# Kernel tuning notes

Measured on AMD Instinct MI355X. Metric: run time of the kernel, lower is better.

## Reference

```python
import jax, jax.numpy as jnp
import numpy as np
import math

HEADS = 32
GROUPS = 8
HEAD_DIM = 64
HIDDEN = 2048
B, S = 2, 2048


def _rope(x, freqs_cis):
    # x: (..., S, head_dim); freqs_cis: (S, head_dim) -> interleaved cos/sin pattern
    x_even = x[..., ::2]
    x_odd = x[..., 1::2]
    cos = freqs_cis[..., ::2]
    sin = freqs_cis[..., 1::2]
    r_even = x_even * cos - x_odd * sin
    r_odd = x_even * sin + x_odd * cos
    return jnp.stack([r_even, r_odd], axis=-1).reshape(x.shape)


def setup_inputs() -> dict:
    key = jax.random.key(0)
    ks = jax.random.split(key, 12)
    scale = 1.0 / math.sqrt(HIDDEN)
    x = jax.random.normal(ks[0], (B, S, HIDDEN), dtype=jnp.float32)
    freqs_cis = jax.random.uniform(ks[1], (S, HEAD_DIM), dtype=jnp.float32)
    causal = jnp.tril(jnp.ones((S, S), dtype=bool))
    mask = jnp.where(causal, 0.0, -1e9).astype(jnp.float32)
    kv_dims = HEAD_DIM * GROUPS
    wq = jax.random.normal(ks[2], (HIDDEN, HIDDEN), jnp.float32) * scale
    bq = jnp.zeros((HIDDEN,), jnp.float32)
    wk = jax.random.normal(ks[3], (kv_dims, HIDDEN), jnp.float32) * scale
    bk = jnp.zeros((kv_dims,), jnp.float32)
    wv = jax.random.normal(ks[4], (kv_dims, HIDDEN), jnp.float32) * scale
    bv = jnp.zeros((kv_dims,), jnp.float32)
    wo = jax.random.normal(ks[5], (HIDDEN, HIDDEN), jnp.float32) * scale
    bo = jnp.zeros((HIDDEN,), jnp.float32)
    return dict(x=x, freqs_cis=freqs_cis, mask=mask, wq=wq, bq=bq,
                wk=wk, bk=bk, wv=wv, bv=bv, wo=wo, bo=bo)


def reference(x, freqs_cis, mask, wq, bq, wk, bk, wv, bv, wo, bo):
    b, s, h = x.shape
    rep = HEADS // GROUPS
    q = x @ wq.T + bq                      # (B,S,H)
    k = x @ wk.T + bk                      # (B,S,G*hd)
    v = x @ wv.T + bv
    q = q.reshape(b, s, HEADS, HEAD_DIM).transpose(0, 2, 1, 3)   # (B,Hh,S,hd)
    k = k.reshape(b, s, GROUPS, HEAD_DIM).transpose(0, 2, 1, 3)  # (B,G,S,hd)
    v = v.reshape(b, s, GROUPS, HEAD_DIM).transpose(0, 2, 1, 3)
    q = _rope(q, freqs_cis)
    k = _rope(k, freqs_cis)
    # GQA: group q heads instead of materially repeating K/V
    qg = q.reshape(b, GROUPS, rep, s, HEAD_DIM)
    scores = jnp.einsum('bgrsd,bgtd->bgrst', qg, k) / math.sqrt(HEAD_DIM)
    scores = scores + mask                 # broadcast (S,S)
    attn = jax.nn.softmax(scores, axis=-1)
    out = jnp.einsum('bgrst,bgtd->bgrsd', attn, v)
    out = out.reshape(b, HEADS, s, HEAD_DIM).transpose(0, 2, 1, 3).reshape(b, s, h)
    return out @ wo.T + bo
```

## Files before the change

### kernel.cpp

```cpp
#include <hip/hip_runtime.h>

#define S_LEN 2048
#define HID   2048
#define NQH   32
#define NKV   8
#define HD    64

typedef __bf16 bf16x8 __attribute__((ext_vector_type(8)));
typedef __bf16 bf16x4 __attribute__((ext_vector_type(4)));
typedef float  f32x4  __attribute__((ext_vector_type(4)));

#define MFMA16(a, b, c) __builtin_amdgcn_mfma_f32_16x16x32_bf16(a, b, c, 0, 0, 0)

__device__ __forceinline__ void async_copy16(const void* g, void* l) {
  __builtin_amdgcn_global_load_lds(
      (const __attribute__((address_space(1))) unsigned int*)g,
      (__attribute__((address_space(3))) unsigned int*)l, 16, 0, 0);
}

__global__ void cast_all_k(const float* __restrict__ x,  const float* __restrict__ wq,
                           const float* __restrict__ wk, const float* __restrict__ wv,
                           const float* __restrict__ wo,
                           __bf16* __restrict__ xb,  __bf16* __restrict__ wqb,
                           __bf16* __restrict__ wkb, __bf16* __restrict__ wvb,
                           __bf16* __restrict__ wob) {
  int bid = blockIdx.x;
  const float* in; __bf16* out; int base;
  if (bid < 8192)       { in = x;  out = xb;  base = bid; }
  else if (bid < 12288) { in = wq; out = wqb; base = bid - 8192; }
  else if (bid < 13312) { in = wk; out = wkb; base = bid - 12288; }
  else if (bid < 14336) { in = wv; out = wvb; base = bid - 13312; }
  else                  { in = wo; out = wob; base = bid - 14336; }
  int i = (base * 256 + threadIdx.x) * 4;
  float4 v = *(const float4*)(in + i);
  bf16x4 o;
  o[0] = (__bf16)v.x; o[1] = (__bf16)v.y; o[2] = (__bf16)v.z; o[3] = (__bf16)v.w;
  *(bf16x4*)(out + i) = o;
}

__device__ __forceinline__ void gemm_core(const __bf16* __restrict__ A, const __bf16* __restrict__ B,
                                          int m0, int n0, int K,
                                          __bf16 (&Asm)[128][32], __bf16 (&Bsm)[128][32],
                                          f32x4 (&acc)[4][4]) {
  const int tid = threadIdx.x, wave = tid >> 6, lane = tid & 63;
  const int l15 = lane & 15, quad = lane >> 4;
  const int wr = wave >> 1, wc = wave & 1;
  const int lrow = lane >> 2, lcol = (lane & 3) * 8;

  const __bf16* ag = A + (size_t)(m0 + wave * 32 + lrow) * K + lcol;
  const __bf16* bg = B + (size_t)(n0 + wave * 32 + lrow) * K + lcol;
  __bf16* al = &Asm[wave * 32][0];
  __bf16* bl = &Bsm[wave * 32][0];
  const size_t rowstep = (size_t)16 * K;

  for (int kt = 0; kt < K; kt += 32) {
    __syncthreads();
    async_copy16(ag + kt, al);
    async_copy16(ag + kt + rowstep, al + 16 * 32);
    async_copy16(bg + kt, bl);
    async_copy16(bg + kt + rowstep, bl + 16 * 32);
    __syncthreads();
    bf16x8 af[4], bfr[4];
#pragma unroll
    for (int mt = 0; mt < 4; mt++)
      af[mt] = *(const bf16x8*)&Asm[wr * 64 + mt * 16 + l15][quad * 8];
#pragma unroll
    for (int nt = 0; nt < 4; nt++)
      bfr[nt] = *(const bf16x8*)&Bsm[wc * 64 + nt * 16 + l15][quad * 8];
#pragma unroll
    for (int mt = 0; mt < 4; mt++)
#pragma unroll
      for (int nt = 0; nt < 4; nt++)
        acc[mt][nt] = MFMA16(af[mt], bfr[nt], acc[mt][nt]);
  }
}

__global__ __launch_bounds__(256) void gemm_qkv_k(const __bf16* __restrict__ xb,
    const __bf16* __restrict__ wqb, const __bf16* __restrict__ wkb, const __bf16* __restrict__ wvb,
    const float* __restrict__ bq, const float* __restrict__ bk, const float* __restrict__ bv,
    const float* __restrict__ fr,
    __bf16* __restrict__ Qb, __bf16* __restrict__ Kb, __bf16* __restrict__ Vt) {
  __shared__ __align__(16) __bf16 Asm[128][32];
  __shared__ __align__(16) __bf16 Bsm[128][32];
  const int by = blockIdx.y;
  const int m0 = blockIdx.x * 128;
  const __bf16* B; const float* bias; int n0;
  int mode;
  if (by < 16)      { B = wqb; bias = bq; n0 = by * 128;        mode = 0; }
  else if (by < 20) { B = wkb; bias = bk; n0 = (by - 16) * 128; mode = 1; }
  else              { B = wvb; bias = bv; n0 = (by - 20) * 128; mode = 2; }

  f32x4 acc[4][4] = {};
  gemm_core(xb, B, m0, n0, HID, Asm, Bsm, acc);

  const int tid = threadIdx.x, wave = tid >> 6, lane = tid & 63;
  const int l15 = lane & 15, quad = lane >> 4;
  const int wr = wave >> 1, wc = wave & 1;

  if (mode == 2) {
#pragma unroll
    for (int nt = 0; nt < 4; nt++) {
      int col = n0 + wc * 64 + nt * 16 + l15;
      int g = col >> 6, d = col & 63;
      float bv2 = bias[col];
#pragma unroll
      for (int mt = 0; mt < 4; mt++) {
        int row = m0 + wr * 64 + mt * 16 + quad * 4;
        int b = row >> 11, s = row & 2047;
        bf16x4 o;
#pragma unroll
        for (int r = 0; r < 4; r++) o[r] = (__bf16)(acc[mt][nt][r] + bv2);
        *(bf16x4*)(Vt + (((size_t)(b * NKV + g) * HD + d)) * S_LEN + s) = o;
      }
    }
  } else {
    const float scale = (mode == 0) ? 0.125f * 1.44269504f : 1.0f;
    const int ldc = (mode == 0) ? HID : 512;
    __bf16* C = (mode == 0) ? Qb : Kb;
    const int dpar = l15 & 1;
#pragma unroll
    for (int nt = 0; nt < 4; nt++) {
      int col = n0 + wc * 64 + nt * 16 + l15;
      int d = col & 63;
      float bv2 = bias[col];
#pragma unroll
      for (int mt = 0; mt < 4; mt++) {
        int row = m0 + wr * 64 + mt * 16 + quad * 4;
        int s = row & 2047;
#pragma unroll
        for (int r = 0; r < 4; r++) {
          float v = acc[mt][nt][r] + bv2;
          float p = __shfl_xor(v, 1, 64);
          float f = fr[(size_t)(s + r) * HD + d];
          float fp = __shfl_xor(f, 1, 64);
          float o = dpar ? (p * f + v * fp) : (v * f - p * fp);
          C[(size_t)(row + r) * ldc + col] = (__bf16)(o * scale);
        }
      }
    }
  }
}

__global__ __launch_bounds__(256) void gemm_out_k(const __bf16* __restrict__ A,
    const __bf16* __restrict__ Bw, const float* __restrict__ bias, float* __restrict__ C) {
  __shared__ __align__(16) __bf16 Asm[128][32];
  __shared__ __align__(16) __bf16 Bsm[128][32];
  const int m0 = blockIdx.x * 128, n0 = blockIdx.y * 128;
  f32x4 acc[4][4] = {};
  gemm_core(A, Bw, m0, n0, HID, Asm, Bsm, acc);
  const int tid = threadIdx.x, wave = tid >> 6, lane = tid & 63;
  const int l15 = lane & 15, quad = lane >> 4;
  const int wr = wave >> 1, wc = wave & 1;
#pragma unroll
  for (int nt = 0; nt < 4; nt++) {
    int col = n0 + wc * 64 + nt * 16 + l15;
    float bv = bias[col];
#pragma unroll
    for (int mt = 0; mt < 4; mt++) {
      int row = m0 + wr * 64 + mt * 16 + quad * 4;
#pragma unroll
      for (int r = 0; r < 4; r++)
        C[(size_t)(row + r) * HID + col] = acc[mt][nt][r] + bv;
    }
  }
}

__global__ __launch_bounds__(256) void flash_k(const __bf16* __restrict__ Q,
                                               const __bf16* __restrict__ K,
                                               const __bf16* __restrict__ Vt,
                                               __bf16* __restrict__ O) {
  __shared__ __align__(64) __bf16 Ksm[64][64];
  __shared__ __align__(64) __bf16 Vsm[64][64];
  __shared__ __align__(64) __bf16 Psm[4][32][64];
  const int tid = threadIdx.x;
  const int wave = tid >> 6, lane = tid & 63;
  const int l15 = lane & 15, quad = lane >> 4;
  const int x7 = l15 & 7, l15h = l15 >> 3;
  const int bh = blockIdx.x;
  const int qt = 15 - blockIdx.y;
  const int b = bh >> 5, h = bh & 31, g = h >> 2;
  const int wq0 = qt * 128 + wave * 32;

  bf16x8 qf[2][2];
#pragma unroll
  for (int mt = 0; mt < 2; mt++) {
    const __bf16* qp = Q + ((size_t)(b * S_LEN + wq0 + mt * 16 + l15)) * HID + h * HD + quad * 8;
    qf[mt][0] = *(const bf16x8*)qp;
    qf[mt][1] = *(const bf16x8*)(qp + 32);
  }
  bf16x8 ones;
#pragma unroll
  for (int j = 0; j < 8; j++) ones[j] = (__bf16)1.0f;

  f32x4 acc[2][4] = {};
  f32x4 accs[2] = {};

  const int srow = tid >> 2, sc = (tid & 3) * 16;
  const int r7 = srow & 7;
  const int w0 = (((sc >> 3))     ^ r7) * 8;
  const int w1 = (((sc >> 3) + 1) ^ r7) * 8;

  char* kbp = (char*)&Ksm[0][0];
  char* vbp = (char*)&Vsm[0][0];
  char* pbp = (char*)&Psm[0][0][0];
  int kr[2], pr[2], pw[4];
#pragma unroll
  for (int ks = 0; ks < 2; ks++) {
    kr[ks] = l15 * 128 + (((ks * 4 + quad) ^ x7) * 16);
    pr[ks] = wave * 4096 + kr[ks];
  }
#pragma unroll
  for (int nt = 0; nt < 4; nt++)
    pw[nt] = wave * 4096 + quad * 512 + x7 * 2 + (((2 * nt + l15h) ^ ((quad & 1) * 4)) * 16);

  const __bf16* kp = K + ((size_t)b * S_LEN + srow) * (NKV * HD) + g * HD + sc;
  const __bf16* vp = Vt + (((size_t)b * NKV + g) * HD + srow) * S_LEN + sc;
  uint4 k0 = *(const uint4*)kp, k1 = *(const uint4*)(kp + 8);
  uint4 v0 = *(const uint4*)vp, v1 = *(const uint4*)(vp + 8);

  const int tmax = 2 * qt + 1;
  for (int t = 0; t <= tmax; t++) {
    const int kv0 = t * 64;
    __syncthreads();
    *(uint4*)&Ksm[srow][w0] = k0;
    *(uint4*)&Ksm[srow][w1] = k1;
    *(uint4*)&Vsm[srow][w0] = v0;
    *(uint4*)&Vsm[srow][w1] = v1;
    if (t < tmax) {
      kp += 64 * NKV * HD;  vp += 64;
      k0 = *(const uint4*)kp; k1 = *(const uint4*)(kp + 8);
      v0 = *(const uint4*)vp; v1 = *(const uint4*)(vp + 8);
    }
    __syncthreads();

    if (kv0 > wq0 + 31) continue;

    bf16x8 kf[2][4];
#pragma unroll
    for (int ks = 0; ks < 2; ks++)
#pragma unroll
      for (int nt = 0; nt < 4; nt++)
        kf[ks][nt] = *(const bf16x8*)(kbp + (kr[ks] + nt * 2048));

    const bool domask = (kv0 + 63 > wq0);
#pragma unroll
    for (int mt = 0; mt < 2; mt++) {
      f32x4 sacc[4] = {};
#pragma unroll
      for (int nt = 0; nt < 4; nt++) {
        sacc[nt] = MFMA16(qf[mt][0], kf[0][nt], sacc[nt]);
        sacc[nt] = MFMA16(qf[mt][1], kf[1][nt], sacc[nt]);
      }
#pragma unroll
      for (int nt = 0; nt < 4; nt++) {
        int kv = kv0 + nt * 16 + l15;
        int qr = wq0 + mt * 16 + quad * 4;
#pragma unroll
        for (int r = 0; r < 4; r++) {
          float p = __builtin_exp2f(sacc[nt][r]);
          if (domask && kv > qr + r) p = 0.f;
          *(__bf16*)(pbp + ((pw[nt] ^ (r << 4)) + (mt * 2048 + r * 128))) = (__bf16)p;
        }
      }
    }

#pragma unroll
    for (int ks = 0; ks < 2; ks++) {
      bf16x8 vf[4];
#pragma unroll
      for (int nt = 0; nt < 4; nt++)
        vf[nt] = *(const bf16x8*)(vbp + (kr[ks] + nt * 2048));
#pragma unroll
      for (int mt = 0; mt < 2; mt++) {
        bf16x8 pf = *(const bf16x8*)(pbp + (pr[ks] + mt * 2048));
        accs[mt] = MFMA16(pf, ones, accs[mt]);
#pragma unroll
        for (int nt = 0; nt < 4; nt++)
          acc[mt][nt] = MFMA16(pf, vf[nt], acc[mt][nt]);
      }
    }
  }

#pragma unroll
  for (int mt = 0; mt < 2; mt++) {
    __bf16* op = O + ((size_t)(b * S_LEN + wq0 + mt * 16 + quad * 4)) * HID + h * HD;
    float inv[4];
#pragma unroll
    for (int r = 0; r < 4; r++) inv[r] = 1.f / accs[mt][r];
#pragma unroll
    for (int nt = 0; nt < 4; nt++)
#pragma unroll
      for (int r = 0; r < 4; r++)
        op[(size_t)r * HID + nt * 16 + l15] = (__bf16)(acc[mt][nt][r] * inv[r]);
  }
}

extern "C" void kernel_launch(void* const* d_in, const int* in_sizes, int n_in,
                              void* d_out, int out_size, void* d_ws, size_t ws_size,
                              hipStream_t stream) {
  (void)in_sizes; (void)n_in; (void)out_size; (void)ws_size;
  const float* x  = (const float*)d_in[0];
  const float* fr = (const float*)d_in[1];
  const float* wq = (const float*)d_in[3];
  const float* bq = (const float*)d_in[4];
  const float* wk = (const float*)d_in[5];
  const float* bk = (const float*)d_in[6];
  const float* wv = (const float*)d_in[7];
  const float* bv = (const float*)d_in[8];
  const float* wo = (const float*)d_in[9];
  const float* bo = (const float*)d_in[10];
  float* out = (float*)d_out;
  char* ws = (char*)d_ws;

  __bf16* xb  = (__bf16*)(ws);
  __bf16* wqb = (__bf16*)(ws + ((size_t)16 << 20));
  __bf16* wkb = (__bf16*)(ws + ((size_t)24 << 20));
  __bf16* wvb = (__bf16*)(ws + ((size_t)26 << 20));
  __bf16* wob = (__bf16*)(ws + ((size_t)28 << 20));
  __bf16* Qb  = (__bf16*)(ws + ((size_t)36 << 20));
  __bf16* Kb  = (__bf16*)(ws + ((size_t)52 << 20));
  __bf16* Vtb = (__bf16*)(ws + ((size_t)60 << 20));
  __bf16* Ab  = (__bf16*)(ws + ((size_t)64 << 20));

  cast_all_k<<<18432, 256, 0, stream>>>(x, wq, wk, wv, wo, xb, wqb, wkb, wvb, wob);

  gemm_qkv_k<<<dim3(32, 24), 256, 0, stream>>>(xb, wqb, wkb, wvb, bq, bk, bv, fr, Qb, Kb, Vtb);

  flash_k<<<dim3(64, 16), 256, 0, stream>>>(Qb, Kb, Vtb, Ab);

  gemm_out_k<<<dim3(32, 16), 256, 0, stream>>>(Ab, wob, bo, out);
}
```

Baseline: 355.0 us.

## Split flash attention into 64-row query tiles with paired causal halves per block

The flash kernel now gives each wave 16 query rows instead of 32, so each block covers a 64-row query tile. Each block handles two tiles in sequence, tile y and tile 31-y, which pairs a short causal range with a long one to balance work across blocks. The P scratch buffer is halved and launch bounds request 4 blocks per CU to raise occupancy. In exchange, every K/V tile is loaded more times across tiles, each loaded K/V tile feeds fewer MFMAs, and a block now runs two sequential passes. The host launch grid is presumably changed to 16 in y to match.

```diff
diff --git a/kernel.cpp b/kernel.cpp
--- a/kernel.cpp
+++ b/kernel.cpp
@@ -165,35 +165,19 @@
   }
 }
 
-__global__ __launch_bounds__(256) void flash_k(const __bf16* __restrict__ Q,
-                                               const __bf16* __restrict__ K,
-                                               const __bf16* __restrict__ Vt,
-                                               __bf16* __restrict__ O) {
+__global__ __launch_bounds__(256, 4) void flash_k(const __bf16* __restrict__ Q,
+                                                  const __bf16* __restrict__ K,
+                                                  const __bf16* __restrict__ Vt,
+                                                  __bf16* __restrict__ O) {
   __shared__ __align__(64) __bf16 Ksm[64][64];
   __shared__ __align__(64) __bf16 Vsm[64][64];
-  __shared__ __align__(64) __bf16 Psm[4][32][64];
+  __shared__ __align__(64) __bf16 Psm[4][16][64];
   const int tid = threadIdx.x;
   const int wave = tid >> 6, lane = tid & 63;
   const int l15 = lane & 15, quad = lane >> 4;
   const int x7 = l15 & 7, l15h = l15 >> 3;
   const int bh = blockIdx.x;
-  const int qt = 15 - blockIdx.y;
   const int b = bh >> 5, h = bh & 31, g = h >> 2;
-  const int wq0 = qt * 128 + wave * 32;
-
-  bf16x8 qf[2][2];
-#pragma unroll
-  for (int mt = 0; mt < 2; mt++) {
-    const __bf16* qp = Q + ((size_t)(b * S_LEN + wq0 + mt * 16 + l15)) * HID + h * HD + quad * 8;
-    qf[mt][0] = *(const bf16x8*)qp;
-    qf[mt][1] = *(const bf16x8*)(qp + 32);
-  }
-  bf16x8 ones;
-#pragma unroll
-  for (int j = 0; j < 8; j++) ones[j] = (__bf16)1.0f;
-
-  f32x4 acc[2][4] = {};
-  f32x4 accs[2] = {};
 
   const int srow = tid >> 2, sc = (tid & 3) * 16;
   const int r7 = srow & 7;
@@ -207,91 +191,101 @@
 #pragma unroll
   for (int ks = 0; ks < 2; ks++) {
     kr[ks] = l15 * 128 + (((ks * 4 + quad) ^ x7) * 16);
-    pr[ks] = wave * 4096 + kr[ks];
+    pr[ks] = wave * 2048 + kr[ks];
   }
 #pragma unroll
   for (int nt = 0; nt < 4; nt++)
-    pw[nt] = wave * 4096 + quad * 512 + x7 * 2 + (((2 * nt + l15h) ^ ((quad & 1) * 4)) * 16);
-
-  const __bf16* kp = K + ((size_t)b * S_LEN + srow) * (NKV * HD) + g * HD + sc;
-  const __bf16* vp = Vt + (((size_t)b * NKV + g) * HD + srow) * S_LEN + sc;
-  uint4 k0 = *(const uint4*)kp, k1 = *(const uint4*)(kp + 8);
-  uint4 v0 = *(const uint4*)vp, v1 = *(const uint4*)(vp + 8);
-
-  const int tmax = 2 * qt + 1;
-  for (int t = 0; t <= tmax; t++) {
-    const int kv0 = t * 64;
-    __syncthreads();
-    *(uint4*)&Ksm[srow][w0] = k0;
-    *(uint4*)&Ksm[srow][w1] = k1;
-    *(uint4*)&Vsm[srow][w0] = v0;
-    *(uint4*)&Vsm[srow][w1] = v1;
-    if (t < tmax) {
-      kp += 64 * NKV * HD;  vp += 64;
-      k0 = *(const uint4*)kp; k1 = *(const uint4*)(kp + 8);
-      v0 = *(const uint4*)vp; v1 = *(const uint4*)(vp + 8);
-    }
-    __syncthreads();
-
-    if (kv0 > wq0 + 31) continue;
-
-    bf16x8 kf[2][4];
-#pragma unroll
-    for (int ks = 0; ks < 2; ks++)
-#pragma unroll
-      for (int nt = 0; nt < 4; nt++)
-        kf[ks][nt] = *(const bf16x8*)(kbp + (kr[ks] + nt * 2048));
-
-    const bool domask = (kv0 + 63 > wq0);
-#pragma unroll
-    for (int mt = 0; mt < 2; mt++) {
+    pw[nt] = wave * 2048 + quad * 512 + x7 * 2 + (((2 * nt + l15h) ^ ((quad & 1) * 4)) * 16);
+
+  bf16x8 ones;
+#pragma unroll
+  for (int j = 0; j < 8; j++) ones[j] = (__bf16)1.0f;
+
+  const __bf16* kbase = K + ((size_t)b * S_LEN + srow) * (NKV * HD) + g * HD + sc;
+  const __bf16* vbase = Vt + (((size_t)b * NKV + g) * HD + srow) * S_LEN + sc;
+
+#pragma unroll 1
+  for (int half = 0; half < 2; half++) {
+    const int qt = half ? (31 - (int)blockIdx.y) : (int)blockIdx.y;
+    const int wq0 = qt * 64 + wave * 16;
+
+    const __bf16* qp = Q + ((size_t)(b * S_LEN + wq0 + l15)) * HID + h * HD + quad * 8;
+    bf16x8 qf0 = *(const bf16x8*)qp;
+    bf16x8 qf1 = *(const bf16x8*)(qp + 32);
+
+    f32x4 acc[4] = {};
+    f32x4 accs = {};
+
+    const __bf16* kp = kbase;
+    const __bf16* vp = vbase;
+    uint4 k0 = *(const uint4*)kp, k1 = *(const uint4*)(kp + 8);
+    uint4 v0 = *(const uint4*)vp, v1 = *(const uint4*)(vp + 8);
+
+    for (int t = 0; t <= qt; t++) {
+      const int kv0 = t * 64;
+      __syncthreads();
+      *(uint4*)&Ksm[srow][w0] = k0;
+      *(uint4*)&Ksm[srow][w1] = k1;
+      *(uint4*)&Vsm[srow][w0] = v0;
+      *(uint4*)&Vsm[srow][w1] = v1;
+      if (t < qt) {
+        kp += 64 * NKV * HD;  vp += 64;
+        k0 = *(const uint4*)kp; k1 = *(const uint4*)(kp + 8);
+        v0 = *(const uint4*)vp; v1 = *(const uint4*)(vp + 8);
+      }
+      __syncthreads();
+
+      if (kv0 > wq0 + 15) continue;
+
+      bf16x8 kf[2][4];
+#pragma unroll
+      for (int ks = 0; ks < 2; ks++)
+#pragma unroll
+        for (int nt = 0; nt < 4; nt++)
+          kf[ks][nt] = *(const bf16x8*)(kbp + (kr[ks] + nt * 2048));
+
       f32x4 sacc[4] = {};
 #pragma unroll
       for (int nt = 0; nt < 4; nt++) {
-        sacc[nt] = MFMA16(qf[mt][0], kf[0][nt], sacc[nt]);
-        sacc[nt] = MFMA16(qf[mt][1], kf[1][nt], sacc[nt]);
-      }
+        sacc[nt] = MFMA16(qf0, kf[0][nt], sacc[nt]);
+        sacc[nt] = MFMA16(qf1, kf[1][nt], sacc[nt]);
+      }
+      const bool domask = (kv0 + 63 > wq0);
 #pragma unroll
       for (int nt = 0; nt < 4; nt++) {
         int kv = kv0 + nt * 16 + l15;
-        int qr = wq0 + mt * 16 + quad * 4;
+        int qr = wq0 + quad * 4;
 #pragma unroll
         for (int r = 0; r < 4; r++) {
           float p = __builtin_exp2f(sacc[nt][r]);
           if (domask && kv > qr + r) p = 0.f;
-          *(__bf16*)(pbp + ((pw[nt] ^ (r << 4)) + (mt * 2048 + r * 128))) = (__bf16)p;
+          *(__bf16*)(pbp + ((pw[nt] ^ (r << 4)) + r * 128)) = (__bf16)p;
         }
       }
+
+#pragma unroll
+      for (int ks = 0; ks < 2; ks++) {
+        bf16x8 vf[4];
+#pragma unroll
+        for (int nt = 0; nt < 4; nt++)
+          vf[nt] = *(const bf16x8*)(vbp + (kr[ks] + nt * 2048));
+        bf16x8 pf = *(const bf16x8*)(pbp + pr[ks]);
+        accs = MFMA16(pf, ones, accs);
+#pragma unroll
+        for (int nt = 0; nt < 4; nt++)
+          acc[nt] = MFMA16(pf, vf[nt], acc[nt]);
+      }
     }
 
-#pragma unroll
-    for (int ks = 0; ks < 2; ks++) {
-      bf16x8 vf[4];
-#pragma unroll
-      for (int nt = 0; nt < 4; nt++)
-        vf[nt] = *(const bf16x8*)(vbp + (kr[ks] + nt * 2048));
-#pragma unroll
-      for (int mt = 0; mt < 2; mt++) {
-        bf16x8 pf = *(const bf16x8*)(pbp + (pr[ks] + mt * 2048));
-        accs[mt] = MFMA16(pf, ones, accs[mt]);
-#pragma unroll
-        for (int nt = 0; nt < 4; nt++)
-          acc[mt][nt] = MFMA16(pf, vf[nt], acc[mt][nt]);
-      }
-    }
-  }
-
-#pragma unroll
-  for (int mt = 0; mt < 2; mt++) {
-    __bf16* op = O + ((size_t)(b * S_LEN + wq0 + mt * 16 + quad * 4)) * HID + h * HD;
+    __bf16* op = O + ((size_t)(b * S_LEN + wq0 + quad * 4)) * HID + h * HD;
     float inv[4];
 #pragma unroll
-    for (int r = 0; r < 4; r++) inv[r] = 1.f / accs[mt][r];
+    for (int r = 0; r < 4; r++) inv[r] = 1.f / accs[r];
 #pragma unroll
     for (int nt = 0; nt < 4; nt++)
 #pragma unroll
       for (int r = 0; r < 4; r++)
-        op[(size_t)r * HID + nt * 16 + l15] = (__bf16)(acc[mt][nt][r] * inv[r]);
+        op[(size_t)r * HID + nt * 16 + l15] = (__bf16)(acc[nt][r] * inv[r]);
   }
 }
 
```

After: 341.9 us. 1.04x faster.
